# Optimization experiments

Hardware: AMD Instinct MI355X
Metric: run time of the kernel (lower is better)

The kernel has to match this reference:

```python
import jax, jax.numpy as jnp
import numpy as np

N_CLASSES = 19


def setup_inputs() -> dict:
    key = jax.random.key(0)
    k1, k2 = jax.random.split(key)
    embedding = jax.random.normal(k1, (4, 32, 128, 128), dtype=jnp.float32)
    label = jax.random.randint(k2, (4, 512, 512), 0, N_CLASSES, dtype=jnp.int64)
    return {"embedding": embedding, "label": label}


def _discriminative_loss(embedding, label, n_classes=N_CLASSES):
    N, H, W = label.shape
    C = embedding.shape[1]
    # bilinear upsample embedding to label resolution (F.upsample mode='bilinear')
    emb = jax.image.resize(embedding, (N, C, H, W), method="bilinear")
    HW = H * W
    emb = emb.reshape(N, C, HW).transpose(0, 2, 1)          # (N, HW, C)
    lab = label.reshape(N, HW)                               # (N, HW)

    onehot = jax.nn.one_hot(lab, n_classes, dtype=emb.dtype)  # (N, HW, K)
    count = onehot.sum(1)                                    # (N, K)
    mask = (count > 0).astype(emb.dtype)                     # (N, K)

    # per-class embedding sum and (biased, /(count+1)) mean
    cls_sum = jnp.einsum("npc,npk->nkc", emb, onehot)       # (N, K, C)
    cls_mean = cls_sum / (count[:, :, None] + 1.0)           # (N, K, C)

    # intra-class: per-pixel squared distance to own-class mean, mean over C
    mean_pp = jnp.take_along_axis(cls_mean, lab[:, :, None], axis=1)  # (N, HW, C)
    d2 = jnp.mean((emb - mean_pp) ** 2, axis=-1)             # (N, HW)
    intra_per_cls = jnp.einsum("np,npk->nk", d2, onehot) / (count + 1.0)  # (N, K)
    n_fg = mask[:, 1:].sum(1)                                # (N,)
    l2_intra = (intra_per_cls[:, 1:] * mask[:, 1:]).sum(1) / n_fg  # (N,)

    # inter-class: pairwise mean squared distance between class means
    diff = cls_mean[:, :, None, :] - cls_mean[:, None, :, :]  # (N, K, K, C)
    inter = jnp.mean(diff ** 2, axis=-1)                     # (N, K, K)
    inter = inter * mask[:, None, :] * mask[:, :, None]
    l2_inter = inter[:, 1:, 1:].reshape(N, -1).sum(1) / (n_fg * n_fg)  # (N,)

    return l2_intra - l2_inter


def reference(embedding, label):
    return _discriminative_loss(embedding, label)
```

## Files before the change

### kernel.cpp

```cpp
#include <hip/hip_runtime.h>

#define NIMG 4
#define NCLS 19
#define CCH  32
#define LH   128
#define LW   128
#define HH   512
#define WW   512
#define HWQ  (LH*LW)
#define HWP  (HH*WW)

#define TR 8
#define TC 16
#define NTX (LW/TC)
#define NTY (LH/TR)
#define NTILE (NTY*NTX)
#define TCELLS (TR*TC)
#define HALO_R (TR*4+4)
#define HALO_C (TC*4+4)

#define NCHUNK 4
#define GPLANES 5

__device__ __forceinline__ void taps(int v, int lim, int& i0, float& w0, float& w1) {
    int r = v & 3;
    int b = (v >> 2) + ((r < 2) ? -1 : 0);
    float f = 0.125f + 0.25f * (float)((r + 2) & 3);
    w0 = 1.f - f; w1 = f;
    if (b < 0)           { b = 0;       w0 = 1.f; w1 = 0.f; }
    else if (b >= lim)   { b = lim - 1; w0 = 0.f; w1 = 1.f; }
    i0 = b;
}

__global__ __launch_bounds__(256) void k_gram(const float* __restrict__ E,
                                              float* __restrict__ G) {
    int n = blockIdx.y;
    int chunk = blockIdx.x >> 6;
    int rp    = blockIdx.x & 63;
    int x  = threadIdx.x & 127;
    int dy = threadIdx.x >> 7;
    int y  = rp * 2 + dy;
    int yp = (y < LH - 1) ? y + 1 : y;
    int xp = (x < LW - 1) ? x + 1 : x;
    bool lane63 = ((x & 63) == 63);
    const float* Ep = E + ((size_t)n * CCH + chunk * 8) * HWQ;
    float g0 = 0.f, g1 = 0.f, g2 = 0.f, g3 = 0.f, g4 = 0.f;
#pragma unroll
    for (int c = 0; c < 8; c++) {
        float a  = Ep[y * LW + x];
        float b  = Ep[yp * LW + x];
        float ar = __shfl_down(a, 1);
        float br = __shfl_down(b, 1);
        if (lane63) { ar = Ep[y * LW + xp]; br = Ep[yp * LW + xp]; }
        g0 = fmaf(a, a,  g0);
        g1 = fmaf(a, ar, g1);
        g2 = fmaf(a, b,  g2);
        g3 = fmaf(a, br, g3);
        g4 = fmaf(ar, b, g4);
        Ep += HWQ;
    }
    float* Gp = G + (((size_t)n * NCHUNK + chunk) * GPLANES) * HWQ + y * LW + x;
    Gp[0]       = g0;
    Gp[HWQ]     = g1;
    Gp[2 * HWQ] = g2;
    Gp[3 * HWQ] = g3;
    Gp[4 * HWQ] = g4;
}

__global__ __launch_bounds__(256) void k_field(const float* __restrict__ E,
        const int* __restrict__ lab, const float* __restrict__ G,
        float* __restrict__ P_sum, float* __restrict__ P_cnt, float* __restrict__ P_S2) {
    int tile = blockIdx.x, n = blockIdx.y;
    int ty = tile >> 3, tx = tile & 7;
    int Y0 = ty * TR, X0 = tx * TC;
    __shared__ float A[TCELLS * NCLS];
    __shared__ float red[8 * NCLS * CCH];
    __shared__ float Gt[4 * 10 * 18];
    __shared__ float S2b[NCLS];
    int tid = threadIdx.x;
    for (int i = tid; i < TCELLS * NCLS; i += 256) A[i] = 0.f;
    if (tid < NCLS) S2b[tid] = 0.f;

    const float* Gn = G + (size_t)n * (NCHUNK * GPLANES * HWQ);
    for (int i = tid; i < 4 * 180; i += 256) {
        int p = i / 180, r = i % 180, gy = r / 18, gx = r % 18;
        int yy = Y0 - 1 + gy; yy = yy < 0 ? 0 : (yy > LH - 1 ? LH - 1 : yy);
        int xx = X0 - 1 + gx; xx = xx < 0 ? 0 : (xx > LW - 1 ? LW - 1 : xx);
        int off = yy * LW + xx;
        float s;
        if (p < 3) {
            s = Gn[(0 * GPLANES + p) * HWQ + off] + Gn[(1 * GPLANES + p) * HWQ + off]
              + Gn[(2 * GPLANES + p) * HWQ + off] + Gn[(3 * GPLANES + p) * HWQ + off];
        } else {
            s = 0.f;
#pragma unroll
            for (int ch = 0; ch < 4; ch++)
                s += Gn[(ch * GPLANES + 3) * HWQ + off] + Gn[(ch * GPLANES + 4) * HWQ + off];
        }
        Gt[i] = s;
    }
    __syncthreads();

    const int* ln = lab + (size_t)n * HWP;
    int h_lo = Y0 * 4 - 2, w_lo = X0 * 4 - 2;
    for (int i = tid; i < HALO_R * HALO_C; i += 256) {
        int hr = i / HALO_C, wc = i - hr * HALO_C;
        int h = h_lo + hr, w = w_lo + wc;
        if (h < 0 || h >= HH || w < 0 || w >= WW) continue;
        int L = ln[h * WW + w];
        int y0, x0; float wy0, wy1, wx0, wx1;
        taps(h, LH - 1, y0, wy0, wy1);
        taps(w, LW - 1, x0, wx0, wx1);
        int ry = y0 - Y0, rx = x0 - X0;
        if (ry >= 0 && ry < TR) {
            if (rx >= 0 && rx < TC)         atomicAdd(&A[(ry * TC + rx) * NCLS + L], wy0 * wx0);
            if (rx + 1 >= 0 && rx + 1 < TC) atomicAdd(&A[(ry * TC + rx + 1) * NCLS + L], wy0 * wx1);
        }
        if (ry + 1 >= 0 && ry + 1 < TR) {
            if (rx >= 0 && rx < TC)         atomicAdd(&A[((ry + 1) * TC + rx) * NCLS + L], wy1 * wx0);
            if (rx + 1 >= 0 && rx + 1 < TC) atomicAdd(&A[((ry + 1) * TC + rx + 1) * NCLS + L], wy1 * wx1);
        }
        if (h >= Y0 * 4 && h < Y0 * 4 + TR * 4 && w >= X0 * 4 && w < X0 * 4 + TC * 4) {
            int gy = y0 - (Y0 - 1), gx = x0 - (X0 - 1);
            int g00 = gy * 18 + gx;
            float u0 = wy0 * wy0, u1 = wy1 * wy1, u2 = wy0 * wy1;
            float s0 = wx0 * wx0, s1 = wx1 * wx1, s2 = wx0 * wx1;
            float d2 =
                u0 * (s0 * Gt[g00]      + s1 * Gt[g00 + 1]  + 2.f * s2 * Gt[180 + g00])
              + u1 * (s0 * Gt[g00 + 18] + s1 * Gt[g00 + 19] + 2.f * s2 * Gt[180 + g00 + 18])
              + 2.f * u2 * (s0 * Gt[360 + g00] + s1 * Gt[360 + g00 + 1] + s2 * Gt[540 + g00]);
            atomicAdd(&S2b[L], d2);
        }
    }
    __syncthreads();

    int g = tid >> 5, c = tid & 31;
    const float* Ec = E + ((size_t)n * CCH + c) * HWQ;
    float acc[NCLS];
#pragma unroll
    for (int k = 0; k < NCLS; k++) acc[k] = 0.f;
#pragma unroll
    for (int j = 0; j < TCELLS / 8; j++) {
        int cell = g * (TCELLS / 8) + j;
        int cy = cell >> 4, cx = cell & 15;
        float e = Ec[(Y0 + cy) * LW + (X0 + cx)];
        const float* Ar = &A[cell * NCLS];
#pragma unroll
        for (int k = 0; k < NCLS; k++) acc[k] = fmaf(Ar[k], e, acc[k]);
    }
#pragma unroll
    for (int k = 0; k < NCLS; k++) red[(g * NCLS + k) * CCH + c] = acc[k];
    __syncthreads();

    float* Ps = P_sum + (size_t)(n * NTILE + tile) * (NCLS * CCH);
    for (int idx = tid; idx < NCLS * CCH; idx += 256) {
        float s = 0.f;
#pragma unroll
        for (int gg = 0; gg < 8; gg++) s += red[gg * NCLS * CCH + idx];
        Ps[idx] = s;
    }
    if (tid < NCLS) {
        float s = 0.f;
        for (int cell = 0; cell < TCELLS; cell++) s += A[cell * NCLS + tid];
        P_cnt[(size_t)(n * NTILE + tile) * NCLS + tid] = s;
        P_S2[(size_t)(n * NTILE + tile) * NCLS + tid] = S2b[tid];
    }
}

__global__ __launch_bounds__(384) void k_final(const float* __restrict__ P_sum,
        const float* __restrict__ P_cnt, const float* __restrict__ P_S2,
        float* __restrict__ out) {
    int n = blockIdx.x, t = threadIdx.x;
    __shared__ float csum[NCLS * 33];
    __shared__ float m[NCLS * 33];
    __shared__ float cnt[NCLS];
    __shared__ float S2[NCLS];
    __shared__ float rk1[NCLS * 17];
    __shared__ float rk2[NCLS * 17];
    __shared__ float sIntra, sNfg, sInter;

    if (t == 0) sInter = 0.f;
    if (t < 304) {
        int k = t >> 4, gg = t & 15;
        const float* p1 = P_cnt + ((size_t)n * NTILE + gg * 8) * NCLS + k;
        const float* p2 = P_S2  + ((size_t)n * NTILE + gg * 8) * NCLS + k;
        float s1 = 0.f, s2 = 0.f;
#pragma unroll
        for (int j = 0; j < 8; j++) { s1 += p1[j * NCLS]; s2 += p2[j * NCLS]; }
        rk1[k * 17 + gg] = s1; rk2[k * 17 + gg] = s2;
    }
    for (int idx = t; idx < NCLS * CCH; idx += 384) {
        float s = 0.f;
        const float* p = P_sum + (size_t)n * NTILE * NCLS * CCH + idx;
        for (int b = 0; b < NTILE; b++) s += p[b * NCLS * CCH];
        csum[(idx >> 5) * 33 + (idx & 31)] = s;
    }
    __syncthreads();
    if (t < NCLS) {
        float s1 = 0.f, s2 = 0.f;
        for (int gg = 0; gg < 16; gg++) { s1 += rk1[t * 17 + gg]; s2 += rk2[t * 17 + gg]; }
        cnt[t] = s1; S2[t] = s2;
    }
    __syncthreads();
    for (int idx = t; idx < NCLS * CCH; idx += 384) {
        int k = idx >> 5, c = idx & 31;
        m[k * 33 + c] = csum[k * 33 + c] / (cnt[k] + 1.f);
    }
    __syncthreads();

    float vi = 0.f, fg = 0.f;
    if (t >= 1 && t < NCLS && cnt[t] > 0.f) {
        fg = 1.f;
        float dot = 0.f, mm = 0.f;
        for (int c = 0; c < CCH; c++) {
            float mv = m[t * 33 + c];
            dot = fmaf(mv, csum[t * 33 + c], dot);
            mm = fmaf(mv, mv, mm);
        }
        vi = (S2[t] - 2.f * dot + cnt[t] * mm) * (1.f / 32.f) / (cnt[t] + 1.f);
    }
#pragma unroll
    for (int s_ = 32; s_ >= 1; s_ >>= 1) { vi += __shfl_xor(vi, s_); fg += __shfl_xor(fg, s_); }
    if (t == 0) { sIntra = vi; sNfg = fg; }

    float ve = 0.f;
    if (t < 324) {
        int j = 1 + t / 18, k = 1 + t % 18;
        if (cnt[j] > 0.f && cnt[k] > 0.f) {
            float s = 0.f;
            for (int c = 0; c < CCH; c++) {
                float d = m[j * 33 + c] - m[k * 33 + c];
                s = fmaf(d, d, s);
            }
            ve = s * (1.f / 32.f);
        }
    }
#pragma unroll
    for (int s_ = 32; s_ >= 1; s_ >>= 1) ve += __shfl_xor(ve, s_);
    if ((t & 63) == 0) atomicAdd(&sInter, ve);
    __syncthreads();
    if (t == 0) out[n] = sIntra / sNfg - sInter / (sNfg * sNfg);
}

extern "C" void kernel_launch(void* const* d_in, const int* in_sizes, int n_in,
                              void* d_out, int out_size, void* d_ws, size_t ws_size,
                              hipStream_t stream) {
    const float* E = (const float*)d_in[0];
    const int* lab = (const int*)d_in[1];
    float* out = (float*)d_out;

    float* ws = (float*)d_ws;
    float* P_sum = ws;
    float* P_cnt = P_sum + (size_t)NIMG * NTILE * NCLS * CCH;
    float* P_S2  = P_cnt + (size_t)NIMG * NTILE * NCLS;
    float* G     = P_S2  + (size_t)NIMG * NTILE * NCLS;

    k_gram <<<dim3(256, NIMG),   dim3(256), 0, stream>>>(E, G);
    k_field<<<dim3(NTILE, NIMG), dim3(256), 0, stream>>>(E, lab, G, P_sum, P_cnt, P_S2);
    k_final<<<dim3(NIMG),        dim3(384), 0, stream>>>(P_sum, P_cnt, P_S2, out);
}
```

Measured before the change: 116.0 us.

## Fuse Gram computation into field kernel and vectorize label scatter

Drops the separate Gram kernel and its global G buffer. Each tile now stages its embedding halo into shared memory and computes the neighbour dot products there. The label pass reads four labels at once as an int4 and uses precomputed x-weights on interior columns, with per-wave S2 accumulators to spread atomic contention. The class-sum reduction now uses shared atomics instead of a reduction buffer, and the final kernel reads partial sums as float4 split across two thread groups. The cost is more shared memory per block and redundant halo loads.

```diff
diff --git a/kernel.cpp b/kernel.cpp
--- a/kernel.cpp
+++ b/kernel.cpp
@@ -16,11 +16,10 @@
 #define NTY (LH/TR)
 #define NTILE (NTY*NTX)
 #define TCELLS (TR*TC)
-#define HALO_R (TR*4+4)
-#define HALO_C (TC*4+4)
-
-#define NCHUNK 4
-#define GPLANES 5
+
+#define PRR 11
+#define PCC 19
+#define PSTR (PRR*PCC)
 
 __device__ __forceinline__ void taps(int v, int lim, int& i0, float& w0, float& w1) {
     int r = v & 3;
@@ -32,138 +31,187 @@
     i0 = b;
 }
 
-__global__ __launch_bounds__(256) void k_gram(const float* __restrict__ E,
-                                              float* __restrict__ G) {
-    int n = blockIdx.y;
-    int chunk = blockIdx.x >> 6;
-    int rp    = blockIdx.x & 63;
-    int x  = threadIdx.x & 127;
-    int dy = threadIdx.x >> 7;
-    int y  = rp * 2 + dy;
-    int yp = (y < LH - 1) ? y + 1 : y;
-    int xp = (x < LW - 1) ? x + 1 : x;
-    bool lane63 = ((x & 63) == 63);
-    const float* Ep = E + ((size_t)n * CCH + chunk * 8) * HWQ;
-    float g0 = 0.f, g1 = 0.f, g2 = 0.f, g3 = 0.f, g4 = 0.f;
-#pragma unroll
-    for (int c = 0; c < 8; c++) {
-        float a  = Ep[y * LW + x];
-        float b  = Ep[yp * LW + x];
-        float ar = __shfl_down(a, 1);
-        float br = __shfl_down(b, 1);
-        if (lane63) { ar = Ep[y * LW + xp]; br = Ep[yp * LW + xp]; }
-        g0 = fmaf(a, a,  g0);
-        g1 = fmaf(a, ar, g1);
-        g2 = fmaf(a, b,  g2);
-        g3 = fmaf(a, br, g3);
-        g4 = fmaf(ar, b, g4);
-        Ep += HWQ;
-    }
-    float* Gp = G + (((size_t)n * NCHUNK + chunk) * GPLANES) * HWQ + y * LW + x;
-    Gp[0]       = g0;
-    Gp[HWQ]     = g1;
-    Gp[2 * HWQ] = g2;
-    Gp[3 * HWQ] = g3;
-    Gp[4 * HWQ] = g4;
-}
-
 __global__ __launch_bounds__(256) void k_field(const float* __restrict__ E,
-        const int* __restrict__ lab, const float* __restrict__ G,
+        const int* __restrict__ lab,
         float* __restrict__ P_sum, float* __restrict__ P_cnt, float* __restrict__ P_S2) {
     int tile = blockIdx.x, n = blockIdx.y;
     int ty = tile >> 3, tx = tile & 7;
     int Y0 = ty * TR, X0 = tx * TC;
+    __shared__ float Ep[CCH * PSTR];
     __shared__ float A[TCELLS * NCLS];
-    __shared__ float red[8 * NCLS * CCH];
-    __shared__ float Gt[4 * 10 * 18];
-    __shared__ float S2b[NCLS];
+    __shared__ float Gt[4 * 180];
+    __shared__ float cs[NCLS * CCH];
+    __shared__ float S2w[4 * NCLS];
+    __shared__ float tmpc[NCLS * 8];
     int tid = threadIdx.x;
+
     for (int i = tid; i < TCELLS * NCLS; i += 256) A[i] = 0.f;
-    if (tid < NCLS) S2b[tid] = 0.f;
-
-    const float* Gn = G + (size_t)n * (NCHUNK * GPLANES * HWQ);
-    for (int i = tid; i < 4 * 180; i += 256) {
-        int p = i / 180, r = i % 180, gy = r / 18, gx = r % 18;
-        int yy = Y0 - 1 + gy; yy = yy < 0 ? 0 : (yy > LH - 1 ? LH - 1 : yy);
-        int xx = X0 - 1 + gx; xx = xx < 0 ? 0 : (xx > LW - 1 ? LW - 1 : xx);
-        int off = yy * LW + xx;
-        float s;
-        if (p < 3) {
-            s = Gn[(0 * GPLANES + p) * HWQ + off] + Gn[(1 * GPLANES + p) * HWQ + off]
-              + Gn[(2 * GPLANES + p) * HWQ + off] + Gn[(3 * GPLANES + p) * HWQ + off];
+    for (int i = tid; i < NCLS * CCH; i += 256) cs[i] = 0.f;
+    if (tid < 4 * NCLS) S2w[tid] = 0.f;
+    const float* En = E + (size_t)n * CCH * HWQ;
+    for (int i = tid; i < CCH * PSTR; i += 256) {
+        int ch = i / PSTR, rem = i - ch * PSTR;
+        int r = rem / PCC, c = rem - r * PCC;
+        int yy = Y0 - 1 + r; yy = yy < 0 ? 0 : (yy > LH - 1 ? LH - 1 : yy);
+        int xx = X0 - 1 + c; xx = xx < 0 ? 0 : (xx > LW - 1 ? LW - 1 : xx);
+        Ep[i] = En[ch * HWQ + yy * LW + xx];
+    }
+    __syncthreads();
+
+    if (tid < 180) {
+        int gy = tid / 18, gx = tid - gy * 18;
+        int yi = Y0 - 1 + gy; yi = yi < 0 ? 0 : (yi > LH - 1 ? LH - 1 : yi);
+        int xi = X0 - 1 + gx; xi = xi < 0 ? 0 : (xi > LW - 1 ? LW - 1 : xi);
+        int yn = (yi + 1 > LH - 1) ? LH - 1 : yi + 1;
+        int xn = (xi + 1 > LW - 1) ? LW - 1 : xi + 1;
+        int p00 = (yi - Y0 + 1) * PCC + (xi - X0 + 1);
+        int p01 = (yi - Y0 + 1) * PCC + (xn - X0 + 1);
+        int p10 = (yn - Y0 + 1) * PCC + (xi - X0 + 1);
+        int p11 = (yn - Y0 + 1) * PCC + (xn - X0 + 1);
+        float gs = 0.f, gh = 0.f, gv = 0.f, gda = 0.f;
+        const float* ep = Ep;
+#pragma unroll 8
+        for (int ch = 0; ch < CCH; ch++, ep += PSTR) {
+            float a = ep[p00], ar = ep[p01], b = ep[p10], br = ep[p11];
+            gs = fmaf(a, a, gs);
+            gh = fmaf(a, ar, gh);
+            gv = fmaf(a, b, gv);
+            gda = fmaf(a, br, fmaf(ar, b, gda));
+        }
+        Gt[tid] = gs; Gt[180 + tid] = gh; Gt[360 + tid] = gv; Gt[540 + tid] = gda;
+    }
+    __syncthreads();
+
+    const float* Gs_ = Gt, * Gh_ = Gt + 180, * Gv_ = Gt + 360, * Gda_ = Gt + 540;
+    const int* ln = lab + (size_t)n * HWP;
+    int h_lo = Y0 * 4 - 2;
+    for (int i = tid; i < 36 * 18; i += 256) {
+        int hr = i / 18, qi = i - hr * 18;
+        int h = h_lo + hr;
+        int q = X0 - 1 + qi;
+        if (h < 0 || h >= HH || q < 0 || q >= LW) continue;
+        int y0; float wy0, wy1;
+        taps(h, LH - 1, y0, wy0, wy1);
+        int ry = y0 - Y0;
+        bool r0 = (unsigned)ry < (unsigned)TR, r1 = (unsigned)(ry + 1) < (unsigned)TR;
+        int rxm = q - 1 - X0, rx0 = q - X0, rxp = q + 1 - X0;
+        bool bm = (unsigned)rxm < (unsigned)TC, b0 = (unsigned)rx0 < (unsigned)TC,
+             bp = (unsigned)rxp < (unsigned)TC;
+        int4 l4 = *(const int4*)(ln + h * WW + (q << 2));
+        bool fast = (q >= 1) && (q <= 126);
+        bool owned = ((unsigned)(h - Y0 * 4) < 32u) && b0;
+
+        if (fast) {
+            if (r0) {
+                int rb = (ry * TC) * NCLS;
+                if (bm) { float* a = &A[rb + rxm * NCLS];
+                    atomicAdd(a + l4.x, wy0 * 0.375f); atomicAdd(a + l4.y, wy0 * 0.125f); }
+                if (b0) { float* a = &A[rb + rx0 * NCLS];
+                    atomicAdd(a + l4.x, wy0 * 0.625f); atomicAdd(a + l4.y, wy0 * 0.875f);
+                    atomicAdd(a + l4.z, wy0 * 0.875f); atomicAdd(a + l4.w, wy0 * 0.625f); }
+                if (bp) { float* a = &A[rb + rxp * NCLS];
+                    atomicAdd(a + l4.z, wy0 * 0.125f); atomicAdd(a + l4.w, wy0 * 0.375f); }
+            }
+            if (r1) {
+                int rb = ((ry + 1) * TC) * NCLS;
+                if (bm) { float* a = &A[rb + rxm * NCLS];
+                    atomicAdd(a + l4.x, wy1 * 0.375f); atomicAdd(a + l4.y, wy1 * 0.125f); }
+                if (b0) { float* a = &A[rb + rx0 * NCLS];
+                    atomicAdd(a + l4.x, wy1 * 0.625f); atomicAdd(a + l4.y, wy1 * 0.875f);
+                    atomicAdd(a + l4.z, wy1 * 0.875f); atomicAdd(a + l4.w, wy1 * 0.625f); }
+                if (bp) { float* a = &A[rb + rxp * NCLS];
+                    atomicAdd(a + l4.z, wy1 * 0.125f); atomicAdd(a + l4.w, wy1 * 0.375f); }
+            }
+            if (owned) {
+                float u0 = wy0 * wy0, u1 = wy1 * wy1, u2t = 2.f * wy0 * wy1;
+                int g00 = (y0 - Y0 + 1) * 18 + rx0;
+                float C0 = u0 * Gs_[g00]     + u1 * Gs_[g00 + 18] + u2t * Gv_[g00];
+                float C1 = u0 * Gs_[g00 + 1] + u1 * Gs_[g00 + 19] + u2t * Gv_[g00 + 1];
+                float C2 = u0 * Gs_[g00 + 2] + u1 * Gs_[g00 + 20] + u2t * Gv_[g00 + 2];
+                float D0 = 2.f * (u0 * Gh_[g00]     + u1 * Gh_[g00 + 18]) + u2t * Gda_[g00];
+                float D1 = 2.f * (u0 * Gh_[g00 + 1] + u1 * Gh_[g00 + 19]) + u2t * Gda_[g00 + 1];
+                float d2a = fmaf(0.140625f, C0, fmaf(0.390625f, C1, 0.46875f * D0));
+                float d2b = fmaf(0.015625f, C0, fmaf(0.765625f, C1, 0.21875f * D0));
+                float d2c = fmaf(0.765625f, C1, fmaf(0.015625f, C2, 0.21875f * D1));
+                float d2d = fmaf(0.390625f, C1, fmaf(0.140625f, C2, 0.46875f * D1));
+                int wv = (tid >> 6) * NCLS;
+                atomicAdd(&S2w[wv + l4.x], d2a); atomicAdd(&S2w[wv + l4.y], d2b);
+                atomicAdd(&S2w[wv + l4.z], d2c); atomicAdd(&S2w[wv + l4.w], d2d);
+            }
         } else {
-            s = 0.f;
-#pragma unroll
-            for (int ch = 0; ch < 4; ch++)
-                s += Gn[(ch * GPLANES + 3) * HWQ + off] + Gn[(ch * GPLANES + 4) * HWQ + off];
-        }
-        Gt[i] = s;
-    }
-    __syncthreads();
-
-    const int* ln = lab + (size_t)n * HWP;
-    int h_lo = Y0 * 4 - 2, w_lo = X0 * 4 - 2;
-    for (int i = tid; i < HALO_R * HALO_C; i += 256) {
-        int hr = i / HALO_C, wc = i - hr * HALO_C;
-        int h = h_lo + hr, w = w_lo + wc;
-        if (h < 0 || h >= HH || w < 0 || w >= WW) continue;
-        int L = ln[h * WW + w];
-        int y0, x0; float wy0, wy1, wx0, wx1;
-        taps(h, LH - 1, y0, wy0, wy1);
-        taps(w, LW - 1, x0, wx0, wx1);
-        int ry = y0 - Y0, rx = x0 - X0;
-        if (ry >= 0 && ry < TR) {
-            if (rx >= 0 && rx < TC)         atomicAdd(&A[(ry * TC + rx) * NCLS + L], wy0 * wx0);
-            if (rx + 1 >= 0 && rx + 1 < TC) atomicAdd(&A[(ry * TC + rx + 1) * NCLS + L], wy0 * wx1);
-        }
-        if (ry + 1 >= 0 && ry + 1 < TR) {
-            if (rx >= 0 && rx < TC)         atomicAdd(&A[((ry + 1) * TC + rx) * NCLS + L], wy1 * wx0);
-            if (rx + 1 >= 0 && rx + 1 < TC) atomicAdd(&A[((ry + 1) * TC + rx + 1) * NCLS + L], wy1 * wx1);
-        }
-        if (h >= Y0 * 4 && h < Y0 * 4 + TR * 4 && w >= X0 * 4 && w < X0 * 4 + TC * 4) {
-            int gy = y0 - (Y0 - 1), gx = x0 - (X0 - 1);
-            int g00 = gy * 18 + gx;
-            float u0 = wy0 * wy0, u1 = wy1 * wy1, u2 = wy0 * wy1;
-            float s0 = wx0 * wx0, s1 = wx1 * wx1, s2 = wx0 * wx1;
-            float d2 =
-                u0 * (s0 * Gt[g00]      + s1 * Gt[g00 + 1]  + 2.f * s2 * Gt[180 + g00])
-              + u1 * (s0 * Gt[g00 + 18] + s1 * Gt[g00 + 19] + 2.f * s2 * Gt[180 + g00 + 18])
-              + 2.f * u2 * (s0 * Gt[360 + g00] + s1 * Gt[360 + g00 + 1] + s2 * Gt[540 + g00]);
-            atomicAdd(&S2b[L], d2);
-        }
-    }
-    __syncthreads();
-
-    int g = tid >> 5, c = tid & 31;
-    const float* Ec = E + ((size_t)n * CCH + c) * HWQ;
-    float acc[NCLS];
-#pragma unroll
-    for (int k = 0; k < NCLS; k++) acc[k] = 0.f;
-#pragma unroll
-    for (int j = 0; j < TCELLS / 8; j++) {
-        int cell = g * (TCELLS / 8) + j;
-        int cy = cell >> 4, cx = cell & 15;
-        float e = Ec[(Y0 + cy) * LW + (X0 + cx)];
-        const float* Ar = &A[cell * NCLS];
-#pragma unroll
-        for (int k = 0; k < NCLS; k++) acc[k] = fmaf(Ar[k], e, acc[k]);
-    }
-#pragma unroll
-    for (int k = 0; k < NCLS; k++) red[(g * NCLS + k) * CCH + c] = acc[k];
+            int Ls[4] = {l4.x, l4.y, l4.z, l4.w};
+            float u0 = wy0 * wy0, u1 = wy1 * wy1, u2t = 2.f * wy0 * wy1;
+            int gyr = y0 - Y0 + 1;
+            int wv = (tid >> 6) * NCLS;
+#pragma unroll
+            for (int j = 0; j < 4; j++) {
+                int w = (q << 2) + j;
+                int x0; float wx0, wx1;
+                taps(w, LW - 1, x0, wx0, wx1);
+                int rxa = x0 - X0, rxb = rxa + 1;
+                int L = Ls[j];
+                if (r0) {
+                    int rb = (ry * TC) * NCLS;
+                    if ((unsigned)rxa < (unsigned)TC) atomicAdd(&A[rb + rxa * NCLS + L], wy0 * wx0);
+                    if ((unsigned)rxb < (unsigned)TC) atomicAdd(&A[rb + rxb * NCLS + L], wy0 * wx1);
+                }
+                if (r1) {
+                    int rb = ((ry + 1) * TC) * NCLS;
+                    if ((unsigned)rxa < (unsigned)TC) atomicAdd(&A[rb + rxa * NCLS + L], wy1 * wx0);
+                    if ((unsigned)rxb < (unsigned)TC) atomicAdd(&A[rb + rxb * NCLS + L], wy1 * wx1);
+                }
+                if (owned) {
+                    int gg = gyr * 18 + (x0 - X0 + 1);
+                    float Ca = u0 * Gs_[gg]     + u1 * Gs_[gg + 18] + u2t * Gv_[gg];
+                    float Cb = u0 * Gs_[gg + 1] + u1 * Gs_[gg + 19] + u2t * Gv_[gg + 1];
+                    float Dd = 2.f * (u0 * Gh_[gg] + u1 * Gh_[gg + 18]) + u2t * Gda_[gg];
+                    float d2 = wx0 * wx0 * Ca + wx1 * wx1 * Cb + 2.f * wx0 * wx1 * Dd;
+                    atomicAdd(&S2w[wv + L], d2);
+                }
+            }
+        }
+    }
+    __syncthreads();
+
+    {
+        int g = tid >> 5, c = tid & 31;
+        float acc[NCLS];
+#pragma unroll
+        for (int k = 0; k < NCLS; k++) acc[k] = 0.f;
+        const float* epc = Ep + c * PSTR;
+#pragma unroll
+        for (int j = 0; j < TCELLS / 8; j++) {
+            int cell = g * (TCELLS / 8) + j;
+            int cy = cell >> 4, cx = cell & 15;
+            float e = epc[(cy + 1) * PCC + (cx + 1)];
+            const float* Ar = &A[cell * NCLS];
+#pragma unroll
+            for (int k = 0; k < NCLS; k++) acc[k] = fmaf(Ar[k], e, acc[k]);
+        }
+#pragma unroll
+        for (int k = 0; k < NCLS; k++) atomicAdd(&cs[k * CCH + c], acc[k]);
+    }
+    if (tid < 152) {
+        int g8 = tid / NCLS, k = tid - g8 * NCLS;
+        float s = 0.f;
+        const float* Ac = A + g8 * 16 * NCLS + k;
+#pragma unroll
+        for (int j = 0; j < 16; j++) s += Ac[j * NCLS];
+        tmpc[k * 8 + g8] = s;
+    }
+    if (tid < NCLS) {
+        P_S2[(size_t)(n * NTILE + tile) * NCLS + tid] =
+            S2w[tid] + S2w[NCLS + tid] + S2w[2 * NCLS + tid] + S2w[3 * NCLS + tid];
+    }
     __syncthreads();
 
     float* Ps = P_sum + (size_t)(n * NTILE + tile) * (NCLS * CCH);
-    for (int idx = tid; idx < NCLS * CCH; idx += 256) {
-        float s = 0.f;
-#pragma unroll
-        for (int gg = 0; gg < 8; gg++) s += red[gg * NCLS * CCH + idx];
-        Ps[idx] = s;
-    }
+    for (int idx = tid; idx < NCLS * CCH; idx += 256) Ps[idx] = cs[idx];
     if (tid < NCLS) {
         float s = 0.f;
-        for (int cell = 0; cell < TCELLS; cell++) s += A[cell * NCLS + tid];
+#pragma unroll
+        for (int g8 = 0; g8 < 8; g8++) s += tmpc[tid * 8 + g8];
         P_cnt[(size_t)(n * NTILE + tile) * NCLS + tid] = s;
-        P_S2[(size_t)(n * NTILE + tile) * NCLS + tid] = S2b[tid];
     }
 }
 
@@ -177,6 +225,7 @@
     __shared__ float S2[NCLS];
     __shared__ float rk1[NCLS * 17];
     __shared__ float rk2[NCLS * 17];
+    __shared__ float4 p4buf[304];
     __shared__ float sIntra, sNfg, sInter;
 
     if (t == 0) sInter = 0.f;
@@ -189,13 +238,25 @@
         for (int j = 0; j < 8; j++) { s1 += p1[j * NCLS]; s2 += p2[j * NCLS]; }
         rk1[k * 17 + gg] = s1; rk2[k * 17 + gg] = s2;
     }
-    for (int idx = t; idx < NCLS * CCH; idx += 384) {
-        float s = 0.f;
-        const float* p = P_sum + (size_t)n * NTILE * NCLS * CCH + idx;
-        for (int b = 0; b < NTILE; b++) s += p[b * NCLS * CCH];
-        csum[(idx >> 5) * 33 + (idx & 31)] = s;
-    }
-    __syncthreads();
+    if (t < 304) {
+        int bg = t / 152, i4 = t - bg * 152;
+        const float4* p4 = (const float4*)P_sum + (size_t)n * NTILE * 152 + i4;
+        float4 s = make_float4(0.f, 0.f, 0.f, 0.f);
+        for (int b = bg * 64; b < bg * 64 + 64; b++) {
+            float4 v = p4[(size_t)b * 152];
+            s.x += v.x; s.y += v.y; s.z += v.z; s.w += v.w;
+        }
+        p4buf[t] = s;
+    }
+    __syncthreads();
+    if (t < 152) {
+        float4 a = p4buf[t], b = p4buf[152 + t];
+        int k = t >> 3, c0 = (t & 7) * 4;
+        csum[k * 33 + c0]     = a.x + b.x;
+        csum[k * 33 + c0 + 1] = a.y + b.y;
+        csum[k * 33 + c0 + 2] = a.z + b.z;
+        csum[k * 33 + c0 + 3] = a.w + b.w;
+    }
     if (t < NCLS) {
         float s1 = 0.f, s2 = 0.f;
         for (int gg = 0; gg < 16; gg++) { s1 += rk1[t * 17 + gg]; s2 += rk2[t * 17 + gg]; }
@@ -253,9 +314,7 @@
     float* P_sum = ws;
     float* P_cnt = P_sum + (size_t)NIMG * NTILE * NCLS * CCH;
     float* P_S2  = P_cnt + (size_t)NIMG * NTILE * NCLS;
-    float* G     = P_S2  + (size_t)NIMG * NTILE * NCLS;
-
-    k_gram <<<dim3(256, NIMG),   dim3(256), 0, stream>>>(E, G);
-    k_field<<<dim3(NTILE, NIMG), dim3(256), 0, stream>>>(E, lab, G, P_sum, P_cnt, P_S2);
+
+    k_field<<<dim3(NTILE, NIMG), dim3(256), 0, stream>>>(E, lab, P_sum, P_cnt, P_S2);
     k_final<<<dim3(NIMG),        dim3(384), 0, stream>>>(P_sum, P_cnt, P_S2, out);
 }
```

Result: slower. 118.7 us (+2.3%).
